# Performance work log

Measured on AMD Instinct MI355X. Metric: run time of the kernel, lower is better.

The kernel has to match this reference:

```python
import jax, jax.numpy as jnp
import numpy as np

THRESH = 0.05
MAX_PER_IMAGE = 50
NMS_THRESH = 0.3
BBOX_STD = jnp.array([0.1, 0.1, 0.2, 0.2], dtype=jnp.float32)  # TRAIN.BBOX_NORMALIZE_STDS


def _decode_boxes(rois, deltas, im_info):
    """bbox_transform_inv + clip_boxes + rescale. rois [N,5], deltas [N,4C], im_info [3]=(h,w,scale).
    Returns [N,C,4] boxes in original-image coordinates."""
    boxes = rois[:, 1:5]
    w = boxes[:, 2] - boxes[:, 0] + 1.0
    h = boxes[:, 3] - boxes[:, 1] + 1.0
    cx = boxes[:, 0] + 0.5 * w
    cy = boxes[:, 1] + 0.5 * h
    d = deltas.reshape(deltas.shape[0], -1, 4) * BBOX_STD  # [N,C,4] (unnormalize deltas)
    dx, dy, dw, dh = d[..., 0], d[..., 1], d[..., 2], d[..., 3]
    pcx = dx * w[:, None] + cx[:, None]
    pcy = dy * h[:, None] + cy[:, None]
    pw = jnp.exp(dw) * w[:, None]
    ph = jnp.exp(dh) * h[:, None]
    x1 = jnp.clip(pcx - 0.5 * pw, 0.0, im_info[1] - 1.0)
    y1 = jnp.clip(pcy - 0.5 * ph, 0.0, im_info[0] - 1.0)
    x2 = jnp.clip(pcx + 0.5 * pw, 0.0, im_info[1] - 1.0)
    y2 = jnp.clip(pcy + 0.5 * ph, 0.0, im_info[0] - 1.0)
    return jnp.stack([x1, y1, x2, y2], axis=-1) / im_info[2]


def _nms(boxes, scores, valid):
    """Greedy NMS, fixed shapes. boxes [N,4], scores [N], valid bool [N].
    Returns (boxes_sorted [N,4], kept_scores [N] with -inf for dropped)."""
    n = boxes.shape[0]
    masked = jnp.where(valid, scores, -jnp.inf)
    order = jnp.argsort(-masked)
    b = boxes[order]
    s = masked[order]
    v = valid[order]
    x1, y1, x2, y2 = b[:, 0], b[:, 1], b[:, 2], b[:, 3]
    area = (x2 - x1 + 1.0) * (y2 - y1 + 1.0)
    ix1 = jnp.maximum(x1[:, None], x1[None, :])
    iy1 = jnp.maximum(y1[:, None], y1[None, :])
    ix2 = jnp.minimum(x2[:, None], x2[None, :])
    iy2 = jnp.minimum(y2[:, None], y2[None, :])
    iw = jnp.clip(ix2 - ix1 + 1.0, 0.0)
    ih = jnp.clip(iy2 - iy1 + 1.0, 0.0)
    inter = iw * ih
    iou = inter / (area[:, None] + area[None, :] - inter)  # [N,N]

    def step(keep, i):
        suppressed = jnp.any(keep & (iou[:, i] > NMS_THRESH))
        k = v[i] & jnp.logical_not(suppressed)
        return keep.at[i].set(k), k

    keep, _ = jax.lax.scan(step, jnp.zeros((n,), dtype=bool), jnp.arange(n))
    return b, jnp.where(keep, s, -jnp.inf)


def _per_image(rois, cls_prob, bbox_pred, im_info):
    """select_boxes for one image: decode, threshold, per-class NMS, global top max_per_image.
    Returns per-class best box [C-1,4] and best score [C-1] within the capped detection set."""
    boxes = _decode_boxes(rois, bbox_pred, im_info)  # [N,C,4]
    n, c = cls_prob.shape
    fg = c - 1

    def per_class(cb, cs):
        return _nms(cb, cs, cs > THRESH)

    fb, fs = jax.vmap(per_class, in_axes=(1, 1))(boxes[:, 1:, :], cls_prob[:, 1:])  # [C-1,N,4],[C-1,N]
    flat_s = fs.reshape(-1)
    flat_b = fb.reshape(-1, 4)
    topk_s, idx = jax.lax.top_k(flat_s, MAX_PER_IMAGE)  # global cap at max_per_image
    topk_b = flat_b[idx]
    topk_cls = idx // n  # fg class id of each kept detection
    # per-class best among kept detections (used by select_box)
    onehot = topk_cls[:, None] == jnp.arange(fg)[None, :]  # [max,fg]
    per_cls = jnp.where(onehot, topk_s[:, None], -jnp.inf)  # [max,fg]
    best_s = per_cls.max(axis=0)  # [fg]
    best_b = topk_b[per_cls.argmax(axis=0)]  # [fg,4]
    return best_b, best_s


def _select_boxes(rois, cls_prob, bbox_pred, im_infos):
    return jax.lax.map(lambda t: _per_image(*t), (rois, cls_prob, bbox_pred, im_infos))


def _forward(rois_A, cls_prob_A, bbox_pred_A, im_info_A, rois_B, cls_prob_B, bbox_pred_B, im_info_B):
    bA_b, bA_s = _select_boxes(rois_A, cls_prob_A, bbox_pred_A, im_info_A)  # [B,fg,4],[B,fg]
    bB_b, bB_s = _select_boxes(rois_B, cls_prob_B, bbox_pred_B, im_info_B)
    joint = bA_s * bB_s  # class must score well in BOTH images
    cls = jnp.argmax(joint, axis=1)  # [B]
    bidx = jnp.arange(joint.shape[0])
    box_A = jax.lax.stop_gradient(bA_b[bidx, cls])
    box_B = jax.lax.stop_gradient(bB_b[bidx, cls])
    return box_A, box_B


def setup_inputs() -> dict:
    key = jax.random.key(0)
    ks = jax.random.split(key, 6)
    B, N, C = 8, 2000, 21
    H, W = 600.0, 800.0

    def make_rois(k):
        k1, k2 = jax.random.split(k)
        xy = jax.random.uniform(k1, (B, N, 2)) * jnp.array([W - 1.0, H - 1.0])
        wh = jax.random.uniform(k2, (B, N, 2), minval=8.0, maxval=300.0)
        x2y2 = jnp.minimum(xy + wh, jnp.array([W - 1.0, H - 1.0]))
        bidx = jnp.zeros((B, N, 1))
        return jnp.concatenate([bidx, xy, x2y2], axis=-1).astype(jnp.float32)

    rois_A = make_rois(ks[0])
    rois_B = make_rois(ks[1])
    cls_prob_A = jax.nn.softmax(2.0 * jax.random.normal(ks[2], (B, N, C)), axis=-1).astype(jnp.float32)
    cls_prob_B = jax.nn.softmax(2.0 * jax.random.normal(ks[3], (B, N, C)), axis=-1).astype(jnp.float32)
    bbox_pred_A = (0.2 * jax.random.normal(ks[4], (B, N, 4 * C))).astype(jnp.float32)
    bbox_pred_B = (0.2 * jax.random.normal(ks[5], (B, N, 4 * C))).astype(jnp.float32)
    im_info = jnp.tile(jnp.array([[H, W, 1.0]], dtype=jnp.float32), (B, 1))
    return dict(rois_A=rois_A, cls_prob_A=cls_prob_A, bbox_pred_A=bbox_pred_A, im_info_A=im_info,
                rois_B=rois_B, cls_prob_B=cls_prob_B, bbox_pred_B=bbox_pred_B, im_info_B=im_info)


def reference(rois_A, cls_prob_A, bbox_pred_A, im_info_A, rois_B, cls_prob_B, bbox_pred_B, im_info_B):
    return _forward(rois_A, cls_prob_A, bbox_pred_A, im_info_A,
                    rois_B, cls_prob_B, bbox_pred_B, im_info_B)
```

## Files before the change

kernel.cpp:

```cpp
#include <hip/hip_runtime.h>
#include <stdint.h>
#include <math.h>

#define BNTH 256
#define CAP 1024
#define MAXK 50
#define THRESH_F 0.05f
#define NMS_T 0.3f
#define SEGW_MAX 32
#define RMAX 8

__device__ __forceinline__ void decode_box(
    const float* __restrict__ rois, const float* __restrict__ pred,
    float H, float W, float scale,
    int b, int n, int c, int N, int C, float out[4])
{
    const float* r = rois + ((size_t)b * N + n) * 5;
    float bx1 = r[1], by1 = r[2], bx2 = r[3], by2 = r[4];
    float w  = bx2 - bx1 + 1.0f;
    float h  = by2 - by1 + 1.0f;
    float cx = bx1 + 0.5f * w;
    float cy = by1 + 0.5f * h;
    const float* d = pred + ((size_t)b * N + n) * 4 * C + 4 * c;
    float dx = d[0] * 0.1f, dy = d[1] * 0.1f;
    float dw = d[2] * 0.2f, dh = d[3] * 0.2f;
    float pcx = dx * w + cx;
    float pcy = dy * h + cy;
    float pw  = expf(dw) * w;
    float ph  = expf(dh) * h;
    float X1 = fminf(fmaxf(pcx - 0.5f * pw, 0.0f), W - 1.0f);
    float Y1 = fminf(fmaxf(pcy - 0.5f * ph, 0.0f), H - 1.0f);
    float X2 = fminf(fmaxf(pcx + 0.5f * pw, 0.0f), W - 1.0f);
    float Y2 = fminf(fmaxf(pcy + 0.5f * ph, 0.0f), H - 1.0f);
    out[0] = X1 / scale;
    out[1] = Y1 / scale;
    out[2] = X2 / scale;
    out[3] = Y2 / scale;
}

template<int SN>
__device__ __forceinline__ void bitonic_desc(double* kd, int lane)
{
    constexpr int NS = SN / 64;
    #pragma unroll
    for (int k = 2; k <= SN; k <<= 1) {
        #pragma unroll
        for (int j = k >> 1; j >= 1; j >>= 1) {
            if (j >= 64) {
                const int js = j >> 6;
                #pragma unroll
                for (int s = 0; s < NS; ++s) {
                    if ((s & js) == 0) {
                        const int sp = s | js;
                        const bool d = (((s << 6) & k) == 0);
                        const double a = kd[s], bb = kd[sp];
                        kd[s]  = d ? fmax(a, bb) : fmin(a, bb);
                        kd[sp] = d ? fmin(a, bb) : fmax(a, bb);
                    }
                }
            } else {
                #pragma unroll
                for (int s = 0; s < NS; ++s) {
                    const double o = __shfl_xor(kd[s], j);
                    const bool lower = (lane & j) == 0;
                    const bool d = ((((s << 6) | lane) & k) == 0);
                    const bool takeMax = (d == lower);
                    const double mx = fmax(kd[s], o);
                    const double mn = fmin(kd[s], o);
                    kd[s] = takeMax ? mx : mn;
                }
            }
        }
    }
}

__global__ __launch_bounds__(BNTH, 1) void nms_kernel(
    const float* __restrict__ rois_A, const float* __restrict__ cls_A,
    const float* __restrict__ pred_A, const float* __restrict__ info_A,
    const float* __restrict__ rois_B, const float* __restrict__ cls_B,
    const float* __restrict__ pred_B, const float* __restrict__ info_B,
    int Bimg, int N, int C,
    float* __restrict__ kept_scores, int* __restrict__ kcounts,
    float* __restrict__ cls_box, int* __restrict__ sync_counter)
{
    const int FG = C - 1;
    const int bx = blockIdx.x;
    const int st  = bx / (Bimg * FG);
    const int rem = bx % (Bimg * FG);
    const int b = rem / FG;
    const int j = rem % FG;
    const int c = j + 1;
    const int tid = threadIdx.x;
    const int w = tid >> 6;
    const int lane = tid & 63;
    const int SEGW = (N + 63) >> 6;

    if (bx == 0 && tid == 0) *sync_counter = 0;

    const float* rois = st ? rois_B : rois_A;
    const float* cls  = st ? cls_B  : cls_A;
    const float* pred = st ? pred_B : pred_A;
    const float* info = st ? info_B : info_A;

    __shared__ uint64_t segKeys[SEGW_MAX][64];
    __shared__ int segCnt[SEGW_MAX];
    __shared__ int offL[SEGW_MAX + 1];
    __shared__ uint64_t keysL[CAP];
    __shared__ float4 boxL[CAP];
    __shared__ float  sarL[CAP];
    __shared__ float4 keptL[MAXK];

    float scv[RMAX];
    #pragma unroll
    for (int r = 0; r < RMAX; ++r) {
        const int seg = w + 4 * r;
        const int n = seg * 64 + lane;
        scv[r] = 0.0f;
        if (seg < SEGW && n < N)
            scv[r] = cls[((size_t)b * N + n) * C + c];
    }
    #pragma unroll
    for (int r = 0; r < RMAX; ++r) {
        const int seg = w + 4 * r;
        if (seg < SEGW) {
            const int n = seg * 64 + lane;
            const bool val = scv[r] > THRESH_F;
            const uint64_t bal = __ballot(val);
            if (val) {
                const int slot = __popcll(bal & ((1ull << lane) - 1ull));
                segKeys[seg][slot] =
                    ((uint64_t)__float_as_uint(scv[r]) << 32) |
                    (uint32_t)(~(uint32_t)n);
            }
            if (lane == 0) segCnt[seg] = __popcll(bal);
        }
    }
    __syncthreads();

    if (tid < 64) {
        int v = (lane < SEGW) ? segCnt[lane] : 0;
        #pragma unroll
        for (int d = 1; d < 64; d <<= 1) {
            const int o = __shfl_up(v, d);
            if (lane >= d) v += o;
        }
        if (lane < SEGW) offL[lane + 1] = v;
        if (lane == 0) offL[0] = 0;
    }
    __syncthreads();
    const int Mfull = offL[SEGW];
    const int M = Mfull < CAP ? Mfull : CAP;

    for (int i = tid; i < CAP; i += BNTH) {
        uint64_t k = 0ull;
        if (i < M) {
            int lo = 0, hi = SEGW;
            while (hi - lo > 1) {
                const int mid = (lo + hi) >> 1;
                if (offL[mid] <= i) lo = mid; else hi = mid;
            }
            k = segKeys[lo][i - offL[lo]];
        }
        keysL[i] = k;
    }
    __syncthreads();

    if (tid < 64) {
        if (M > 1) {
            if (M <= 512) {
                double kd[8];
                #pragma unroll
                for (int s = 0; s < 8; ++s)
                    kd[s] = __longlong_as_double((long long)keysL[s * 64 + lane]);
                bitonic_desc<512>(kd, lane);
                #pragma unroll
                for (int s = 0; s < 8; ++s)
                    keysL[s * 64 + lane] = (uint64_t)__double_as_longlong(kd[s]);
            } else {
                double kd[16];
                #pragma unroll
                for (int s = 0; s < 16; ++s)
                    kd[s] = __longlong_as_double((long long)keysL[s * 64 + lane]);
                bitonic_desc<1024>(kd, lane);
                #pragma unroll
                for (int s = 0; s < 16; ++s)
                    keysL[s * 64 + lane] = (uint64_t)__double_as_longlong(kd[s]);
            }
        }
    }
    __syncthreads();

    const float H = info[b * 3 + 0];
    const float W = info[b * 3 + 1];
    const float scale = info[b * 3 + 2];
    for (int i = tid; i < M; i += BNTH) {
        const uint64_t u = keysL[i];
        const int n = (int)(~(uint32_t)u);
        float o[4];
        decode_box(rois, pred, H, W, scale, b, n, c, N, C, o);
        boxL[i] = make_float4(o[0], o[1], o[2], o[3]);
        sarL[i] = (o[2] - o[0] + 1.0f) * (o[3] - o[1] + 1.0f);
    }
    __syncthreads();

    if (tid < 64) {
        float* ksc = kept_scores + (size_t)bx * MAXK;
        int kcount = 0;
        float4 cls_best = make_float4(0.f, 0.f, 0.f, 0.f);

        for (int s = 0; s * 64 < M && kcount < MAXK; ++s) {
            const int ii = s * 64 + lane;
            const bool valid = (ii < M);
            float cx1 = 0.f, cy1 = 0.f, cx2 = 0.f, cy2 = 0.f, car = 1.0f, csc = 0.f;
            if (valid) {
                const float4 cb4 = boxL[ii];
                cx1 = cb4.x; cy1 = cb4.y; cx2 = cb4.z; cy2 = cb4.w;
                car = sarL[ii];
                csc = __uint_as_float((uint32_t)(keysL[ii] >> 32));
            }
            bool sup = !valid;
            for (int q = 0; q < kcount; ++q) {
                const float4 kb = keptL[q];
                const float kar = (kb.z - kb.x + 1.0f) * (kb.w - kb.y + 1.0f);
                const float ix1 = fmaxf(kb.x, cx1), iy1 = fmaxf(kb.y, cy1);
                const float ix2 = fminf(kb.z, cx2), iy2 = fminf(kb.w, cy2);
                const float iw = fmaxf(ix2 - ix1 + 1.0f, 0.0f);
                const float ih = fmaxf(iy2 - iy1 + 1.0f, 0.0f);
                const float inter = iw * ih;
                sup = sup || (inter / (kar + car - inter) > NMS_T);
            }
            uint64_t alive = ~__ballot(sup);
            while (alive != 0ull && kcount < MAXK) {
                const int l = __builtin_ctzll(alive);
                const int ki = s * 64 + l;
                const float4 kb = boxL[ki];
                const float kar = sarL[ki];
                if (lane == l) {
                    keptL[kcount] = make_float4(cx1, cy1, cx2, cy2);
                    ksc[kcount] = csc;
                }
                if (kcount == 0) cls_best = kb;
                const float ix1 = fmaxf(kb.x, cx1), iy1 = fmaxf(kb.y, cy1);
                const float ix2 = fminf(kb.z, cx2), iy2 = fminf(kb.w, cy2);
                const float iw = fmaxf(ix2 - ix1 + 1.0f, 0.0f);
                const float ih = fmaxf(iy2 - iy1 + 1.0f, 0.0f);
                const float inter = iw * ih;
                const bool s2 = (inter / (kar + car - inter) > NMS_T);
                alive &= ~__ballot(s2);
                alive &= ~(1ull << l);
                kcount++;
            }
        }

        if (lane == 0) {
            kcounts[bx] = kcount;
            float* cbp = cls_box + (size_t)bx * 4;
            cbp[0] = cls_best.x; cbp[1] = cls_best.y;
            cbp[2] = cls_best.z; cbp[3] = cls_best.w;
        }
    }
}

__global__ __launch_bounds__(64) void select_combine(
    const float* __restrict__ kept_scores, const int* __restrict__ kcounts,
    const float* __restrict__ cls_box,
    const float* __restrict__ rois_A, const float* __restrict__ pred_A,
    const float* __restrict__ info_A,
    const float* __restrict__ rois_B, const float* __restrict__ pred_B,
    const float* __restrict__ info_B,
    int Bimg, int N, int C,
    float* best_s, float* best_b, int* sync_counter, float* __restrict__ out)
{
    const int FG = C - 1;
    const int bx = blockIdx.x;
    const int st = bx / Bimg;
    const int b  = bx % Bimg;
    const int tid = threadIdx.x;

    __shared__ float sk[20][MAXK];
    __shared__ int   skc[20];
    __shared__ float stopv[20];
    __shared__ int   cnt20[20];
    __shared__ int   inflag[20];
    __shared__ float gbox[4];
    __shared__ int   amlast;

    const size_t base = (size_t)bx * FG;
    for (int i = tid; i < FG * MAXK; i += 64)
        sk[i / MAXK][i % MAXK] = kept_scores[base * MAXK + i];
    if (tid < FG) {
        skc[tid] = kcounts[base + tid];
        cnt20[tid] = 0;
    }
    __syncthreads();
    if (tid < FG)
        stopv[tid] = (skc[tid] > 0) ? sk[tid][0] : -INFINITY;
    __syncthreads();

    for (int p = tid; p < FG * FG; p += 64) {
        const int cc = p / FG;
        const int c2 = p % FG;
        const float sc = stopv[cc];
        const int k2 = skc[c2];
        int cnt = 0;
        if (skc[cc] > 0) {
            #pragma unroll 5
            for (int k = 0; k < k2; ++k) {
                const float v = sk[c2][k];
                cnt += ((v > sc) || (v == sc && c2 < cc)) ? 1 : 0;
            }
        }
        if (cnt) atomicAdd(&cnt20[cc], cnt);
    }
    __syncthreads();
    if (tid < FG)
        inflag[tid] = (skc[tid] > 0 && cnt20[tid] < MAXK) ? 1 : 0;
    __syncthreads();

    if (tid == 0) {
        int g = -1;
        float bs = -INFINITY;
        for (int c2 = 0; c2 < FG; ++c2)
            if (skc[c2] > 0 && stopv[c2] > bs) { bs = stopv[c2]; g = c2; }
        if (g >= 0) {
            const float* cbp = cls_box + (base + g) * 4;
            gbox[0] = cbp[0]; gbox[1] = cbp[1]; gbox[2] = cbp[2]; gbox[3] = cbp[3];
        } else {
            const float* rois = st ? rois_B : rois_A;
            const float* pred = st ? pred_B : pred_A;
            const float* info = st ? info_B : info_A;
            float o[4];
            decode_box(rois, pred, info[b * 3], info[b * 3 + 1], info[b * 3 + 2],
                       b, 0, 1, N, C, o);
            gbox[0] = o[0]; gbox[1] = o[1]; gbox[2] = o[2]; gbox[3] = o[3];
        }
    }
    __syncthreads();

    if (tid < FG) {
        const int in = inflag[tid];
        best_s[base + tid] = in ? stopv[tid] : -INFINITY;
        float* ob = best_b + (base + tid) * 4;
        if (in) {
            const float* cbp = cls_box + (base + tid) * 4;
            ob[0] = cbp[0]; ob[1] = cbp[1]; ob[2] = cbp[2]; ob[3] = cbp[3];
        } else {
            ob[0] = gbox[0]; ob[1] = gbox[1]; ob[2] = gbox[2]; ob[3] = gbox[3];
        }
    }

    __threadfence();
    if (tid == 0) amlast = (atomicAdd(sync_counter, 1) == 2 * Bimg - 1);
    __syncthreads();
    if (amlast) {
        __threadfence();
        if (tid < Bimg) {
            const int i = tid;
            const float* sA = best_s + (size_t)i * FG;
            const float* sB = best_s + (size_t)(Bimg + i) * FG;
            float bj = 0.0f;
            int cls = 0;
            for (int cc = 0; cc < FG; ++cc) {
                const float v = sA[cc] * sB[cc];
                if (cc == 0 || v > bj) { bj = v; cls = cc; }
            }
            const float* bA = best_b + ((size_t)i * FG + cls) * 4;
            const float* bB = best_b + ((size_t)(Bimg + i) * FG + cls) * 4;
            for (int k = 0; k < 4; ++k) {
                out[i * 4 + k]            = bA[k];
                out[Bimg * 4 + i * 4 + k] = bB[k];
            }
        }
    }
}

extern "C" void kernel_launch(void* const* d_in, const int* in_sizes, int n_in,
                              void* d_out, int out_size, void* d_ws, size_t ws_size,
                              hipStream_t stream) {
    const float* rois_A = (const float*)d_in[0];
    const float* cls_A  = (const float*)d_in[1];
    const float* pred_A = (const float*)d_in[2];
    const float* info_A = (const float*)d_in[3];
    const float* rois_B = (const float*)d_in[4];
    const float* cls_B  = (const float*)d_in[5];
    const float* pred_B = (const float*)d_in[6];
    const float* info_B = (const float*)d_in[7];
    float* out = (float*)d_out;

    const int Bimg = in_sizes[3] / 3;
    const int N    = in_sizes[0] / (Bimg * 5);
    const int C    = in_sizes[1] / (Bimg * N);
    const int FG   = C - 1;
    const int NSB  = 2 * Bimg * FG;

    char* ws = (char*)d_ws;
    int* sync_counter = (int*)ws;
    size_t off = 256;
    float* kept_scores = (float*)(ws + off);
    off += (size_t)NSB * MAXK * sizeof(float);
    int* kcounts = (int*)(ws + off);
    off += (size_t)NSB * sizeof(int);
    float* cls_box = (float*)(ws + off);
    off += (size_t)NSB * 4 * sizeof(float);
    float* best_s = (float*)(ws + off);
    off += (size_t)NSB * sizeof(float);
    float* best_b = (float*)(ws + off);

    nms_kernel<<<NSB, BNTH, 0, stream>>>(
        rois_A, cls_A, pred_A, info_A,
        rois_B, cls_B, pred_B, info_B,
        Bimg, N, C, kept_scores, kcounts, cls_box, sync_counter);

    select_combine<<<2 * Bimg, 64, 0, stream>>>(
        kept_scores, kcounts, cls_box,
        rois_A, pred_A, info_A, rois_B, pred_B, info_B,
        Bimg, N, C, best_s, best_b, sync_counter, out);
}
```

Before: 58.65 us.

## Overlap box decoding with bitonic sort and binary-search per-class rank counts

```diff
diff --git a/kernel.cpp b/kernel.cpp
--- a/kernel.cpp
+++ b/kernel.cpp
@@ -106,9 +106,11 @@
     __shared__ int segCnt[SEGW_MAX];
     __shared__ int offL[SEGW_MAX + 1];
     __shared__ uint64_t keysL[CAP];
+    __shared__ unsigned short rowsL[CAP];
     __shared__ float4 boxL[CAP];
-    __shared__ float  sarL[CAP];
     __shared__ float4 keptL[MAXK];
+
+    float4* boxS = (float4*)segKeys;
 
     float scv[RMAX];
     #pragma unroll
@@ -159,11 +161,17 @@
                 const int mid = (lo + hi) >> 1;
                 if (offL[mid] <= i) lo = mid; else hi = mid;
             }
-            k = segKeys[lo][i - offL[lo]];
+            const uint64_t u = segKeys[lo][i - offL[lo]];
+            rowsL[i] = (unsigned short)(~(uint32_t)u);
+            k = (u & 0xFFFFFFFF00000000ull) | (uint32_t)(~(uint32_t)i);
         }
         keysL[i] = k;
     }
     __syncthreads();
+
+    const float H = info[b * 3 + 0];
+    const float W = info[b * 3 + 1];
+    const float scale = info[b * 3 + 2];
 
     if (tid < 64) {
         if (M > 1) {
@@ -187,19 +195,19 @@
                     keysL[s * 64 + lane] = (uint64_t)__double_as_longlong(kd[s]);
             }
         }
-    }
-    __syncthreads();
-
-    const float H = info[b * 3 + 0];
-    const float W = info[b * 3 + 1];
-    const float scale = info[b * 3 + 2];
+    } else {
+        for (int i = tid - 64; i < M; i += BNTH - 64) {
+            const int n = rowsL[i];
+            float o[4];
+            decode_box(rois, pred, H, W, scale, b, n, c, N, C, o);
+            boxL[i] = make_float4(o[0], o[1], o[2], o[3]);
+        }
+    }
+    __syncthreads();
+
     for (int i = tid; i < M; i += BNTH) {
-        const uint64_t u = keysL[i];
-        const int n = (int)(~(uint32_t)u);
-        float o[4];
-        decode_box(rois, pred, H, W, scale, b, n, c, N, C, o);
-        boxL[i] = make_float4(o[0], o[1], o[2], o[3]);
-        sarL[i] = (o[2] - o[0] + 1.0f) * (o[3] - o[1] + 1.0f);
+        const int slot = (int)(~(uint32_t)keysL[i]) & (CAP - 1);
+        boxS[i] = boxL[slot];
     }
     __syncthreads();
 
@@ -213,9 +221,9 @@
             const bool valid = (ii < M);
             float cx1 = 0.f, cy1 = 0.f, cx2 = 0.f, cy2 = 0.f, car = 1.0f, csc = 0.f;
             if (valid) {
-                const float4 cb4 = boxL[ii];
+                const float4 cb4 = boxS[ii];
                 cx1 = cb4.x; cy1 = cb4.y; cx2 = cb4.z; cy2 = cb4.w;
-                car = sarL[ii];
+                car = (cx2 - cx1 + 1.0f) * (cy2 - cy1 + 1.0f);
                 csc = __uint_as_float((uint32_t)(keysL[ii] >> 32));
             }
             bool sup = !valid;
@@ -233,8 +241,8 @@
             while (alive != 0ull && kcount < MAXK) {
                 const int l = __builtin_ctzll(alive);
                 const int ki = s * 64 + l;
-                const float4 kb = boxL[ki];
-                const float kar = sarL[ki];
+                const float4 kb = boxS[ki];
+                const float kar = (kb.z - kb.x + 1.0f) * (kb.w - kb.y + 1.0f);
                 if (lane == l) {
                     keptL[kcount] = make_float4(cx1, cy1, cx2, cy2);
                     ksc[kcount] = csc;
@@ -303,12 +311,16 @@
         const float sc = stopv[cc];
         const int k2 = skc[c2];
         int cnt = 0;
-        if (skc[cc] > 0) {
-            #pragma unroll 5
-            for (int k = 0; k < k2; ++k) {
-                const float v = sk[c2][k];
-                cnt += ((v > sc) || (v == sc && c2 < cc)) ? 1 : 0;
-            }
+        if (skc[cc] > 0 && k2 > 0) {
+            const float* lp = &sk[c2][0];
+            int lo = 0, hi = k2;
+            while (lo < hi) {
+                const int mid = (lo + hi) >> 1;
+                const float v = lp[mid];
+                const bool greater = (v > sc) || (v == sc && c2 < cc);
+                if (greater) lo = mid + 1; else hi = mid;
+            }
+            cnt = lo;
         }
         if (cnt) atomicAdd(&cnt20[cc], cnt);
     }
```

After: 52.32 us. 10.8% less time.
